# Kernel tuning notes

Measured on AMD Instinct MI355X. Metric: run time of the kernel, lower is better.

## Reference

```python
import jax, jax.numpy as jnp
import numpy as np

RADIUS = 2.0  # ball-query radius (float forward arg in the original; fixed here)


def _conv1x1(x, W, b):
    # 1x1 Conv2D over NHWC == per-point linear layer
    return jnp.einsum('bmsc,cd->bmsd', x, W) + b


def _ball_query(xyz, new_xyz, radius, nsample):
    """For each cluster center, take the first (by index) nsample points within
    radius, padding with the first found neighbor (TF ball-query semantics).
    xyz: (B,N,3), new_xyz: (B,M,3) -> idx (B,M,nsample) int32."""
    N = xyz.shape[1]
    d2 = jnp.sum((new_xyz[:, :, None, :] - xyz[:, None, :, :]) ** 2, axis=-1)  # (B,M,N)
    valid = d2 < radius * radius
    key = jnp.where(valid, jnp.arange(N, dtype=jnp.int32)[None, None, :], N)
    order = jnp.argsort(key, axis=-1)[..., :nsample]          # (B,M,nsample)
    skey = jnp.take_along_axis(key, order, axis=-1)
    idx = jnp.where(skey < N, order, order[..., :1])          # pad with first neighbor
    return idx


def setup_inputs() -> dict:
    key = jax.random.key(0)
    ks = jax.random.split(key, 8)
    B, N = 8, 8192
    xyz = jax.random.normal(ks[0], (B, N, 3), dtype=jnp.float32)

    def w(k, cin, cout):
        return (jax.random.normal(k, (cin, cout), dtype=jnp.float32) / np.sqrt(cin)).astype(jnp.float32)

    z = lambda c: jnp.zeros((c,), jnp.float32)
    inp = {
        'xyz': xyz,
        'W1': w(ks[1], 3, 64),    'b1': z(64),
        'W2': w(ks[2], 64, 128),  'b2': z(128),
        'W3': w(ks[3], 128, 256), 'b3': z(256),
        'W4': w(ks[4], 256, 128), 'b4': z(128),
        'W5': w(ks[5], 128, 64),  'b5': z(64),
        'Wa': w(ks[6], 64, 1),    'ba': z(1),
        'Wo': w(ks[7], 64, 2),    'bo': z(2),
        'num_clusters': 512,
        'num_samples': 64,
    }
    return inp


def reference(xyz, W1, b1, W2, b2, W3, b3, W4, b4, W5, b5, Wa, ba, Wo, bo,
              num_clusters, num_samples):
    # sample cluster centers (deterministic stand-in for random subsampling)
    new_xyz = xyz[:, :num_clusters]                                    # (B,M,3)
    idx = _ball_query(xyz, new_xyz, RADIUS, num_samples)               # (B,M,S)
    grouped = jax.vmap(lambda pts, i: pts[i])(xyz, idx)                # (B,M,S,3)
    g = (grouped - new_xyz[:, :, None, :]) / RADIUS                    # normalize_radius

    # shared per-point MLP (1x1 convs, relu)
    h = jax.nn.relu(_conv1x1(g, W1, b1))
    h = jax.nn.relu(_conv1x1(h, W2, b2))
    h = jax.nn.relu(_conv1x1(h, W3, b3))
    # MaxPoolAxis: max over samples, keepdims
    h = jnp.max(h, axis=2, keepdims=True)                              # (B,M,1,256)
    # mlp2 convs (linear, no activation in source)
    h = _conv1x1(h, W4, b4)
    h = _conv1x1(h, W5, b5)                                            # (B,M,1,64)

    attention = jax.nn.softplus(_conv1x1(h, Wa, ba))[:, :, 0, 0]       # (B,M)
    o = _conv1x1(h, Wo, bo)[:, :, 0, :]                                # (B,M,2)
    o = o / jnp.sqrt(jnp.maximum(jnp.sum(o * o, axis=-1, keepdims=True), 1e-8))
    orientation = jnp.arctan2(o[..., 1], o[..., 0])                    # (B,M)
    return new_xyz, idx, attention, orientation
```

## Files before the change

### kernel.cpp

```cpp
#include <hip/hip_runtime.h>
#include <math.h>

#define BB 8
#define NN 8192
#define MM 512
#define SS 64

#define OUT_IDX   (BB*MM*3)
#define OUT_ATT   (OUT_IDX + BB*MM*SS)
#define OUT_ORI   (OUT_ATT + BB*MM)

typedef short v8s __attribute__((ext_vector_type(8)));
typedef float v4f __attribute__((ext_vector_type(4)));

static __device__ __forceinline__ unsigned short f2bf(float x) {
    unsigned int u = __float_as_uint(x);
    u += 0x7FFFu + ((u >> 16) & 1u);
    return (unsigned short)(u >> 16);
}

__global__ void pack_weights(const float* __restrict__ W2,
                             const float* __restrict__ W3,
                             unsigned short* __restrict__ ws)
{
    const int gid = blockIdx.x * 256 + threadIdx.x;
    const float* W; unsigned short* dst; int N, kt, nt, lane;
    if (gid < 1024) {
        W = W2; N = 128;
        const int tile = gid >> 6; lane = gid & 63;
        kt = tile >> 3; nt = tile & 7;
        dst = ws + (size_t)(tile * 64 + lane) * 8;
    } else {
        const int g = gid - 1024;
        W = W3; N = 256;
        const int tile = g >> 6; lane = g & 63;
        kt = tile >> 4; nt = tile & 15;
        dst = ws + 8192 + (size_t)(tile * 64 + lane) * 8;
    }
    const int k0 = kt * 32 + (lane >> 4) * 8;
    const int n  = nt * 16 + (lane & 15);
    union { unsigned short u[8]; v8s v; } f;
    #pragma unroll
    for (int j = 0; j < 8; ++j) f.u[j] = f2bf(W[(k0 + j) * N + n]);
    *(v8s*)dst = f.v;
}

__global__ __launch_bounds__(256, 3) void feat3d_main(
    const float* __restrict__ xyz,
    const float* __restrict__ W1, const float* __restrict__ b1,
    const float* __restrict__ b2, const float* __restrict__ b3,
    const float* __restrict__ W4, const float* __restrict__ b4,
    const float* __restrict__ W5, const float* __restrict__ b5,
    const float* __restrict__ Wa, const float* __restrict__ ba,
    const float* __restrict__ Wo, const float* __restrict__ bo,
    const unsigned short* __restrict__ Wp,
    float* __restrict__ out)
{
    __shared__ __align__(16) unsigned short a2p[8 * 64 * 8];
    __shared__ __align__(16) unsigned short a3p[16 * 64 * 8];
    __shared__ __align__(16) float smallf[512];
    __shared__ int ls_idx[SS];
    __shared__ unsigned long long ls_mask[4];

    float* ls_g  = smallf;
    float* ls_w1 = smallf + 256;
    float* ls_v  = smallf;
    float* ls_h4 = smallf + 256;
    float* ls_h5 = smallf + 384;

    const int t   = threadIdx.x;
    const int wv  = t >> 6;
    const int l   = t & 63;
    const int q   = l >> 4;
    const int r16 = l & 15;
    const int blk = blockIdx.x;
    const int b   = blk >> 9;
    const int m   = blk & 511;
    const float* xb = xyz + (size_t)b * (NN * 3);

    const float cx = xb[m*3+0], cy = xb[m*3+1], cz = xb[m*3+2];

    if (t < 3) out[(b*MM + m)*3 + t] = xb[m*3 + t];

    {
        int cnt = 0, base = 0, firstIdx = -1;
        while (base < NN && cnt < SS) {
            const int j = base + t;
            const float dx = xb[j*3+0] - cx;
            const float dy = xb[j*3+1] - cy;
            const float dz = xb[j*3+2] - cz;
            const float d2 = __fadd_rn(__fadd_rn(__fmul_rn(dx,dx), __fmul_rn(dy,dy)),
                                       __fmul_rn(dz,dz));
            const bool valid = d2 < 4.0f;
            const unsigned long long mask = __ballot(valid);
            if (l == 0) ls_mask[wv] = mask;
            __syncthreads();
            const unsigned long long m0 = ls_mask[0], m1 = ls_mask[1],
                                     m2 = ls_mask[2], m3 = ls_mask[3];
            int below = __popcll(mask & ((1ull << l) - 1ull));
            if (wv > 0) below += (int)__popcll(m0);
            if (wv > 1) below += (int)__popcll(m1);
            if (wv > 2) below += (int)__popcll(m2);
            const int pos = cnt + below;
            if (valid && pos < SS) ls_idx[pos] = j;
            if (firstIdx < 0) {
                if      (m0) firstIdx = base +       (int)__builtin_ctzll(m0);
                else if (m1) firstIdx = base +  64 + (int)__builtin_ctzll(m1);
                else if (m2) firstIdx = base + 128 + (int)__builtin_ctzll(m2);
                else if (m3) firstIdx = base + 192 + (int)__builtin_ctzll(m3);
            }
            cnt += (int)(__popcll(m0) + __popcll(m1) + __popcll(m2) + __popcll(m3));
            if (cnt > SS) cnt = SS;
            base += 256;
            __syncthreads();
        }
        if (t < SS && t >= cnt) ls_idx[t] = firstIdx;
    }
    __syncthreads();

    if (t < 64) {
        const int p = ls_idx[t];
        out[OUT_IDX + (b*MM + m)*SS + t] = (float)p;
        ls_g[t*4+0] = (xb[p*3+0] - cx) * 0.5f;
        ls_g[t*4+1] = (xb[p*3+1] - cy) * 0.5f;
        ls_g[t*4+2] = (xb[p*3+2] - cz) * 0.5f;
        ls_g[t*4+3] = 0.f;
        ls_w1[t*4+0] = W1[t];
        ls_w1[t*4+1] = W1[64 + t];
        ls_w1[t*4+2] = W1[128 + t];
        ls_w1[t*4+3] = b1[t];
    }
    __syncthreads();

    {
        const int s = wv*16 + r16;
        const float4 g4 = *(const float4*)&ls_g[s*4];
        #pragma unroll
        for (int kt = 0; kt < 2; ++kt) {
            union { unsigned short u[8]; v8s v; } fr;
            #pragma unroll
            for (int j = 0; j < 8; ++j) {
                const int c = kt*32 + q*8 + j;
                const float4 w = *(const float4*)&ls_w1[c*4];
                const float h = fmaf(g4.x, w.x, fmaf(g4.y, w.y, fmaf(g4.z, w.z, w.w)));
                fr.u[j] = f2bf(fmaxf(h, 0.f));
            }
            *(v8s*)&a2p[((kt*4 + wv)*64 + l)*8] = fr.v;
        }
    }
    __syncthreads();

    {
        const v8s* W2f = (const v8s*)Wp;
        v8s bfr[2][2];
        #pragma unroll
        for (int kt = 0; kt < 2; ++kt)
            #pragma unroll
            for (int ni = 0; ni < 2; ++ni)
                bfr[kt][ni] = W2f[(kt*8 + 2*wv + ni)*64 + l];

        const v4f z = {0.f, 0.f, 0.f, 0.f};
        v4f acc[4][2];
        #pragma unroll
        for (int mt = 0; mt < 4; ++mt) { acc[mt][0] = z; acc[mt][1] = z; }

        #pragma unroll
        for (int kt = 0; kt < 2; ++kt)
            #pragma unroll
            for (int mt = 0; mt < 4; ++mt) {
                const v8s a = *(const v8s*)&a2p[((kt*4 + mt)*64 + l)*8];
                #pragma unroll
                for (int ni = 0; ni < 2; ++ni)
                    acc[mt][ni] = __builtin_amdgcn_mfma_f32_16x16x32_bf16(
                        a, bfr[kt][ni], acc[mt][ni], 0, 0, 0);
            }

        #pragma unroll
        for (int ni = 0; ni < 2; ++ni) {
            const int c2  = (2*wv + ni)*16 + r16;
            const float bias = b2[c2];
            const int kt3 = c2 >> 5;
            const int lhi = ((c2 >> 3) & 3) << 4;
            const int j3  = c2 & 7;
            #pragma unroll
            for (int mt = 0; mt < 4; ++mt)
                #pragma unroll
                for (int rg = 0; rg < 4; ++rg) {
                    const float h = fmaxf(acc[mt][ni][rg] + bias, 0.f);
                    const int s15 = q*4 + rg;
                    a3p[((kt3*4 + mt)*64 + (lhi | s15))*8 + j3] = f2bf(h);
                }
        }
    }
    __syncthreads();

    {
        const v8s* W3f = (const v8s*)(Wp + 8192);
        const v4f z = {0.f, 0.f, 0.f, 0.f};
        v4f acc[4][4];
        #pragma unroll
        for (int mt = 0; mt < 4; ++mt)
            #pragma unroll
            for (int ni = 0; ni < 4; ++ni) acc[mt][ni] = z;

        #pragma unroll
        for (int kt = 0; kt < 4; ++kt) {
            v8s a[4], bb[4];
            #pragma unroll
            for (int mt = 0; mt < 4; ++mt)
                a[mt] = *(const v8s*)&a3p[((kt*4 + mt)*64 + l)*8];
            #pragma unroll
            for (int ni = 0; ni < 4; ++ni)
                bb[ni] = W3f[(kt*16 + 4*wv + ni)*64 + l];
            #pragma unroll
            for (int mt = 0; mt < 4; ++mt)
                #pragma unroll
                for (int ni = 0; ni < 4; ++ni)
                    acc[mt][ni] = __builtin_amdgcn_mfma_f32_16x16x32_bf16(
                        a[mt], bb[ni], acc[mt][ni], 0, 0, 0);
        }

        #pragma unroll
        for (int ni = 0; ni < 4; ++ni) {
            float mx = acc[0][ni][0];
            #pragma unroll
            for (int mt = 0; mt < 4; ++mt)
                #pragma unroll
                for (int rg = 0; rg < 4; ++rg)
                    mx = fmaxf(mx, acc[mt][ni][rg]);
            mx = fmaxf(mx, __shfl_xor(mx, 16));
            mx = fmaxf(mx, __shfl_xor(mx, 32));
            if (q == 0) {
                const int c = (4*wv + ni)*16 + r16;
                ls_v[c] = fmaxf(mx + b3[c], 0.f);
            }
        }
    }
    __syncthreads();

    if (t < 128) {
        float acc = b4[t];
        #pragma unroll 8
        for (int k = 0; k < 256; ++k)
            acc = fmaf(ls_v[k], W4[k*128 + t], acc);
        ls_h4[t] = acc;
    }
    __syncthreads();

    if (t < 64) {
        float acc = b5[t];
        #pragma unroll 8
        for (int k = 0; k < 128; ++k)
            acc = fmaf(ls_h4[k], W5[k*64 + t], acc);
        ls_h5[t] = acc;
    }
    __syncthreads();

    if (t < 64) {
        const float hv = ls_h5[t];
        float va = hv * Wa[t];
        float v0 = hv * Wo[2*t + 0];
        float v1 = hv * Wo[2*t + 1];
        #pragma unroll
        for (int off = 32; off > 0; off >>= 1) {
            va += __shfl_down(va, off);
            v0 += __shfl_down(v0, off);
            v1 += __shfl_down(v1, off);
        }
        if (t == 0) {
            const float a = va + ba[0];
            const float att = fmaxf(a, 0.f) + log1pf(expf(-fabsf(a)));
            out[OUT_ATT + b*MM + m] = att;
            out[OUT_ORI + b*MM + m] = atan2f(v1 + bo[1], v0 + bo[0]);
        }
    }
}

extern "C" void kernel_launch(void* const* d_in, const int* in_sizes, int n_in,
                              void* d_out, int out_size, void* d_ws, size_t ws_size,
                              hipStream_t stream) {
    const float* xyz = (const float*)d_in[0];
    const float* W1  = (const float*)d_in[1];
    const float* b1  = (const float*)d_in[2];
    const float* W2  = (const float*)d_in[3];
    const float* b2  = (const float*)d_in[4];
    const float* W3  = (const float*)d_in[5];
    const float* b3  = (const float*)d_in[6];
    const float* W4  = (const float*)d_in[7];
    const float* b4  = (const float*)d_in[8];
    const float* W5  = (const float*)d_in[9];
    const float* b5  = (const float*)d_in[10];
    const float* Wa  = (const float*)d_in[11];
    const float* ba  = (const float*)d_in[12];
    const float* Wo  = (const float*)d_in[13];
    const float* bo  = (const float*)d_in[14];

    unsigned short* Wp = (unsigned short*)d_ws;

    pack_weights<<<dim3(20), dim3(256), 0, stream>>>(W2, W3, Wp);
    feat3d_main<<<dim3(BB*MM), dim3(256), 0, stream>>>(
        xyz, W1, b1, b2, b3, W4, b4, W5, b5, Wa, ba, Wo, bo, Wp, (float*)d_out);
}
```

Baseline: 155.7 us.

## Fuse weight packing into main kernel and streamline ball query and MLP tail

Removes the separate weight-packing kernel. Each block now reads W2/W3 directly from fp32 global memory, taking the high 16 bits as a truncated bf16 fragment. The ball-query loop double-buffers its ballot masks to drop one barrier per iteration, and writes normalized offsets directly instead of re-gathering points. The W4 layer is split across all 256 threads, and launch bounds rise to 4 blocks per SM. The risks are strided per-block weight gathers and truncation instead of round-to-nearest, which changes numerics slightly.

```diff
diff --git a/kernel.cpp b/kernel.cpp
--- a/kernel.cpp
+++ b/kernel.cpp
@@ -19,54 +19,29 @@
     return (unsigned short)(u >> 16);
 }
 
-__global__ void pack_weights(const float* __restrict__ W2,
-                             const float* __restrict__ W3,
-                             unsigned short* __restrict__ ws)
-{
-    const int gid = blockIdx.x * 256 + threadIdx.x;
-    const float* W; unsigned short* dst; int N, kt, nt, lane;
-    if (gid < 1024) {
-        W = W2; N = 128;
-        const int tile = gid >> 6; lane = gid & 63;
-        kt = tile >> 3; nt = tile & 7;
-        dst = ws + (size_t)(tile * 64 + lane) * 8;
-    } else {
-        const int g = gid - 1024;
-        W = W3; N = 256;
-        const int tile = g >> 6; lane = g & 63;
-        kt = tile >> 4; nt = tile & 15;
-        dst = ws + 8192 + (size_t)(tile * 64 + lane) * 8;
-    }
-    const int k0 = kt * 32 + (lane >> 4) * 8;
-    const int n  = nt * 16 + (lane & 15);
-    union { unsigned short u[8]; v8s v; } f;
-    #pragma unroll
-    for (int j = 0; j < 8; ++j) f.u[j] = f2bf(W[(k0 + j) * N + n]);
-    *(v8s*)dst = f.v;
-}
-
-__global__ __launch_bounds__(256, 3) void feat3d_main(
+__global__ __launch_bounds__(256, 4) void feat3d_fused(
     const float* __restrict__ xyz,
     const float* __restrict__ W1, const float* __restrict__ b1,
-    const float* __restrict__ b2, const float* __restrict__ b3,
+    const float* __restrict__ W2, const float* __restrict__ b2,
+    const float* __restrict__ W3, const float* __restrict__ b3,
     const float* __restrict__ W4, const float* __restrict__ b4,
     const float* __restrict__ W5, const float* __restrict__ b5,
     const float* __restrict__ Wa, const float* __restrict__ ba,
     const float* __restrict__ Wo, const float* __restrict__ bo,
-    const unsigned short* __restrict__ Wp,
     float* __restrict__ out)
 {
-    __shared__ __align__(16) unsigned short a2p[8 * 64 * 8];
-    __shared__ __align__(16) unsigned short a3p[16 * 64 * 8];
-    __shared__ __align__(16) float smallf[512];
-    __shared__ int ls_idx[SS];
-    __shared__ unsigned long long ls_mask[4];
-
-    float* ls_g  = smallf;
-    float* ls_w1 = smallf + 256;
-    float* ls_v  = smallf;
-    float* ls_h4 = smallf + 256;
-    float* ls_h5 = smallf + 384;
+    __shared__ __align__(16) unsigned char lds[27136];
+    unsigned short* a2p = (unsigned short*)lds;
+    unsigned short* a3p = (unsigned short*)(lds + 8192);
+    float* smallf       = (float*)(lds + 24576);
+    int* ls_idx         = (int*)(lds + 26624);
+    unsigned long long* ls_mask = (unsigned long long*)(lds + 26880);
+
+    float* ls_g   = smallf;
+    float* ls_w1  = smallf + 256;
+    float* ls_v   = smallf;
+    float* ls_par = smallf + 256;
+    float* ls_h5  = (float*)lds;
 
     const int t   = threadIdx.x;
     const int wv  = t >> 6;
@@ -82,8 +57,16 @@
 
     if (t < 3) out[(b*MM + m)*3 + t] = xb[m*3 + t];
 
-    {
-        int cnt = 0, base = 0, firstIdx = -1;
+    if (t < 64) {
+        ls_w1[t*4+0] = W1[t];
+        ls_w1[t*4+1] = W1[64 + t];
+        ls_w1[t*4+2] = W1[128 + t];
+        ls_w1[t*4+3] = b1[t];
+    }
+
+    int cnt = 0;
+    {
+        int base = 0, pb = 0;
         while (base < NN && cnt < SS) {
             const int j = base + t;
             const float dx = xb[j*3+0] - cx;
@@ -93,44 +76,36 @@
                                        __fmul_rn(dz,dz));
             const bool valid = d2 < 4.0f;
             const unsigned long long mask = __ballot(valid);
-            if (l == 0) ls_mask[wv] = mask;
+            if (l == 0) ls_mask[pb*4 + wv] = mask;
             __syncthreads();
-            const unsigned long long m0 = ls_mask[0], m1 = ls_mask[1],
-                                     m2 = ls_mask[2], m3 = ls_mask[3];
+            const unsigned long long m0 = ls_mask[pb*4+0], m1 = ls_mask[pb*4+1],
+                                     m2 = ls_mask[pb*4+2], m3 = ls_mask[pb*4+3];
             int below = __popcll(mask & ((1ull << l) - 1ull));
             if (wv > 0) below += (int)__popcll(m0);
             if (wv > 1) below += (int)__popcll(m1);
             if (wv > 2) below += (int)__popcll(m2);
             const int pos = cnt + below;
-            if (valid && pos < SS) ls_idx[pos] = j;
-            if (firstIdx < 0) {
-                if      (m0) firstIdx = base +       (int)__builtin_ctzll(m0);
-                else if (m1) firstIdx = base +  64 + (int)__builtin_ctzll(m1);
-                else if (m2) firstIdx = base + 128 + (int)__builtin_ctzll(m2);
-                else if (m3) firstIdx = base + 192 + (int)__builtin_ctzll(m3);
+            if (valid && pos < SS) {
+                ls_idx[pos]   = j;
+                ls_g[pos*4+0] = dx * 0.5f;
+                ls_g[pos*4+1] = dy * 0.5f;
+                ls_g[pos*4+2] = dz * 0.5f;
             }
             cnt += (int)(__popcll(m0) + __popcll(m1) + __popcll(m2) + __popcll(m3));
             if (cnt > SS) cnt = SS;
             base += 256;
-            __syncthreads();
-        }
-        if (t < SS && t >= cnt) ls_idx[t] = firstIdx;
-    }
-    __syncthreads();
-
-    if (t < 64) {
-        const int p = ls_idx[t];
-        out[OUT_IDX + (b*MM + m)*SS + t] = (float)p;
-        ls_g[t*4+0] = (xb[p*3+0] - cx) * 0.5f;
-        ls_g[t*4+1] = (xb[p*3+1] - cy) * 0.5f;
-        ls_g[t*4+2] = (xb[p*3+2] - cz) * 0.5f;
-        ls_g[t*4+3] = 0.f;
-        ls_w1[t*4+0] = W1[t];
-        ls_w1[t*4+1] = W1[64 + t];
-        ls_w1[t*4+2] = W1[128 + t];
-        ls_w1[t*4+3] = b1[t];
-    }
-    __syncthreads();
+            pb ^= 1;
+        }
+    }
+    __syncthreads();
+    if (t < SS && t >= cnt) {
+        ls_idx[t]   = ls_idx[0];
+        ls_g[t*4+0] = ls_g[0];
+        ls_g[t*4+1] = ls_g[1];
+        ls_g[t*4+2] = ls_g[2];
+    }
+    __syncthreads();
+    if (t < 64) out[OUT_IDX + (b*MM + m)*SS + t] = (float)ls_idx[t];
 
     {
         const int s = wv*16 + r16;
@@ -151,13 +126,19 @@
     __syncthreads();
 
     {
-        const v8s* W2f = (const v8s*)Wp;
+        const unsigned short* W2h = (const unsigned short*)W2;
         v8s bfr[2][2];
         #pragma unroll
         for (int kt = 0; kt < 2; ++kt)
             #pragma unroll
-            for (int ni = 0; ni < 2; ++ni)
-                bfr[kt][ni] = W2f[(kt*8 + 2*wv + ni)*64 + l];
+            for (int ni = 0; ni < 2; ++ni) {
+                const int c2 = (2*wv + ni)*16 + r16;
+                union { unsigned short u[8]; v8s v; } f;
+                #pragma unroll
+                for (int j = 0; j < 8; ++j)
+                    f.u[j] = W2h[2*((kt*32 + q*8 + j)*128 + c2) + 1];
+                bfr[kt][ni] = f.v;
+            }
 
         const v4f z = {0.f, 0.f, 0.f, 0.f};
         v4f acc[4][2];
@@ -195,7 +176,7 @@
     __syncthreads();
 
     {
-        const v8s* W3f = (const v8s*)(Wp + 8192);
+        const unsigned short* W3h = (const unsigned short*)W3;
         const v4f z = {0.f, 0.f, 0.f, 0.f};
         v4f acc[4][4];
         #pragma unroll
@@ -210,8 +191,14 @@
             for (int mt = 0; mt < 4; ++mt)
                 a[mt] = *(const v8s*)&a3p[((kt*4 + mt)*64 + l)*8];
             #pragma unroll
-            for (int ni = 0; ni < 4; ++ni)
-                bb[ni] = W3f[(kt*16 + 4*wv + ni)*64 + l];
+            for (int ni = 0; ni < 4; ++ni) {
+                const int c3 = (4*wv + ni)*16 + r16;
+                union { unsigned short u[8]; v8s v; } f;
+                #pragma unroll
+                for (int j = 0; j < 8; ++j)
+                    f.u[j] = W3h[2*((kt*32 + q*8 + j)*256 + c3) + 1];
+                bb[ni] = f.v;
+            }
             #pragma unroll
             for (int mt = 0; mt < 4; ++mt)
                 #pragma unroll
@@ -238,12 +225,16 @@
     }
     __syncthreads();
 
-    if (t < 128) {
-        float acc = b4[t];
+    {
+        const int c  = t & 127;
+        const int hf = t >> 7;
+        float acc = hf ? 0.f : b4[c];
+        const float* vsrc = ls_v + hf*128;
+        const float* wsrc = W4 + (size_t)(hf*128)*128 + c;
         #pragma unroll 8
-        for (int k = 0; k < 256; ++k)
-            acc = fmaf(ls_v[k], W4[k*128 + t], acc);
-        ls_h4[t] = acc;
+        for (int k = 0; k < 128; ++k)
+            acc = fmaf(vsrc[k], wsrc[k*128], acc);
+        ls_par[t] = acc;
     }
     __syncthreads();
 
@@ -251,7 +242,7 @@
         float acc = b5[t];
         #pragma unroll 8
         for (int k = 0; k < 128; ++k)
-            acc = fmaf(ls_h4[k], W5[k*64 + t], acc);
+            acc = fmaf(ls_par[k] + ls_par[128 + k], W5[k*64 + t], acc);
         ls_h5[t] = acc;
     }
     __syncthreads();
@@ -295,9 +286,7 @@
     const float* Wo  = (const float*)d_in[13];
     const float* bo  = (const float*)d_in[14];
 
-    unsigned short* Wp = (unsigned short*)d_ws;
-
-    pack_weights<<<dim3(20), dim3(256), 0, stream>>>(W2, W3, Wp);
-    feat3d_main<<<dim3(BB*MM), dim3(256), 0, stream>>>(
-        xyz, W1, b1, b2, b3, W4, b4, W5, b5, Wa, ba, Wo, bo, Wp, (float*)d_out);
+    feat3d_fused<<<dim3(BB*MM), dim3(256), 0, stream>>>(
+        xyz, W1, b1, W2, b2, W3, b3, W4, b4, W5, b5, Wa, ba, Wo, bo,
+        (float*)d_out);
 }
```

After: 193.2 us. 1.24x slower.
